# Performance work log

Measured on AMD Instinct MI355X. Metric: run time of the kernel, lower is better.

## Reference

```python
import jax, jax.numpy as jnp
import numpy as np

N_NODES = 50000
N_EDGES = 1000000
H_DIM = 128
OUT_DIM = 64
N_RELS = 16  # num_bases == num_rels


def setup_inputs() -> dict:
    key = jax.random.key(0)
    ks = jax.random.split(key, 12)
    node_ids = jnp.arange(N_NODES, dtype=jnp.int64) if jax.config.jax_enable_x64 else jnp.arange(N_NODES, dtype=jnp.int32)
    src = jax.random.randint(ks[0], (N_EDGES,), 0, N_NODES)
    dst = jax.random.randint(ks[1], (N_EDGES,), 0, N_NODES)
    etype = jax.random.randint(ks[2], (N_EDGES,), 0, N_RELS)
    norm = jax.random.uniform(ks[3], (N_EDGES, 1), dtype=jnp.float32)
    s1 = 1.0 / np.sqrt(H_DIM)
    s2 = 1.0 / np.sqrt(OUT_DIM)
    emb = jax.random.normal(ks[4], (N_NODES, H_DIM), dtype=jnp.float32)
    V1 = jax.random.normal(ks[5], (N_RELS, H_DIM, H_DIM), dtype=jnp.float32) * s1
    comp1 = jax.random.normal(ks[6], (N_RELS, N_RELS), dtype=jnp.float32) * (1.0 / np.sqrt(N_RELS))
    bias1 = jnp.zeros((H_DIM,), dtype=jnp.float32)
    V2 = jax.random.normal(ks[7], (N_RELS, H_DIM, OUT_DIM), dtype=jnp.float32) * s2
    comp2 = jax.random.normal(ks[8], (N_RELS, N_RELS), dtype=jnp.float32) * (1.0 / np.sqrt(N_RELS))
    bias2 = jnp.zeros((OUT_DIM,), dtype=jnp.float32)
    return {"node_ids": node_ids, "src": src, "dst": dst, "etype": etype, "norm": norm,
            "emb": emb, "V1": V1, "comp1": comp1, "bias1": bias1,
            "V2": V2, "comp2": comp2, "bias2": bias2}


def _rel_graph_conv(x, src, dst, etype, norm, V, comp, bias, num_nodes):
    # Basis decomposition: W_r = sum_b comp[r, b] * V_b  -> [R, in, out]
    W = jnp.einsum('rb,bio->rio', comp, V)
    # Per-relation transform of all nodes: [R, N, out]
    Y = jnp.einsum('ni,rio->rno', x, W)
    # Per-edge message: gather (etype, src) then scale by norm  -> [E, out]
    m = Y[etype, src] * norm
    # Scatter-add to destination nodes
    h = jax.ops.segment_sum(m, dst, num_segments=num_nodes)
    return h + bias


def reference(node_ids, src, dst, etype, norm, emb, V1, comp1, bias1, V2, comp2, bias2):
    x = emb[node_ids]  # [N, H]
    h = jax.nn.relu(_rel_graph_conv(x, src, dst, etype, norm, V1, comp1, bias1, x.shape[0]))
    h = _rel_graph_conv(h, src, dst, etype, norm, V2, comp2, bias2, x.shape[0])
    return h
```

## Files before the change

### kernel.cpp

```cpp
#include <hip/hip_runtime.h>


typedef short bf16x8 __attribute__((ext_vector_type(8)));
typedef float f32x4 __attribute__((ext_vector_type(4)));

#define RELS 16
#define HDIM 128
#define DSTBLK 66
#define MT_P 5
#define CHUNK 32
#define MAXBINS 12288

__device__ inline unsigned short f2bf(float f) {
  unsigned int u = __float_as_uint(f);
  unsigned int r = u + 0x7FFFu + ((u >> 16) & 1u);
  return (unsigned short)(r >> 16);
}

__global__ void cvt_bf16(const float* __restrict__ in, unsigned short* __restrict__ out, int n8) {
  int i = blockIdx.x * blockDim.x + threadIdx.x;
  if (i >= n8) return;
  float4 a = ((const float4*)in)[i * 2];
  float4 b = ((const float4*)in)[i * 2 + 1];
  uint4 o;
  o.x = (unsigned)f2bf(a.x) | ((unsigned)f2bf(a.y) << 16);
  o.y = (unsigned)f2bf(a.z) | ((unsigned)f2bf(a.w) << 16);
  o.z = (unsigned)f2bf(b.x) | ((unsigned)f2bf(b.y) << 16);
  o.w = (unsigned)f2bf(b.z) | ((unsigned)f2bf(b.w) << 16);
  ((uint4*)out)[i] = o;
}

__global__ void compute_w(const float* __restrict__ comp, const float* __restrict__ V,
                          unsigned short* __restrict__ Wt, int IO) {
  int idx = blockIdx.x * blockDim.x + threadIdx.x;
  if (idx >= RELS * IO * HDIM) return;
  int k = idx & (HDIM - 1);
  int o = (idx >> 7) % IO;
  int r = idx / (IO * HDIM);
  float s = 0.f;
#pragma unroll
  for (int b = 0; b < RELS; b++)
    s = fmaf(comp[r * RELS + b], V[(size_t)b * HDIM * IO + (size_t)k * IO + o], s);
  Wt[idx] = f2bf(s);
}

__global__ void hist_bins(const int* __restrict__ dst, const int* __restrict__ etype,
                          int n, int nbins, int* __restrict__ counts) {
  __shared__ int lh[MAXBINS];
  for (int j = threadIdx.x; j < nbins; j += blockDim.x) lh[j] = 0;
  __syncthreads();
  for (int i = blockIdx.x * blockDim.x + threadIdx.x; i < n; i += gridDim.x * blockDim.x)
    atomicAdd(&lh[(dst[i] / DSTBLK) * RELS + etype[i]], 1);
  __syncthreads();
  for (int j = threadIdx.x; j < nbins; j += blockDim.x) {
    int c = lh[j];
    if (c) atomicAdd(&counts[j], c);
  }
}

__global__ void scan_offsets(const int* __restrict__ counts, int* __restrict__ offsets, int nbins) {
  __shared__ int csum[256];
  const int t = threadIdx.x;
  const int CH = (nbins + 255) / 256;
  int lo = t * CH, hi = min(lo + CH, nbins);
  int s = 0;
  for (int i = lo; i < hi; i++) s += (counts[i] + 15) & ~15;
  csum[t] = s;
  __syncthreads();
#pragma unroll
  for (int d = 1; d < 256; d <<= 1) {
    int v = (t >= d) ? csum[t - d] : 0;
    __syncthreads();
    csum[t] += v;
    __syncthreads();
  }
  int run = (t == 0) ? 0 : csum[t - 1];
  for (int i = lo; i < hi; i++) {
    offsets[i] = run;
    run += (counts[i] + 15) & ~15;
  }
  if (lo < nbins && hi == nbins) offsets[nbins] = run;
}

__global__ void scatter_bins(const int* __restrict__ src, const int* __restrict__ dst,
                             const int* __restrict__ etype, const float* __restrict__ norm,
                             int n, const int* __restrict__ offsets, int* __restrict__ cursor,
                             uint2* __restrict__ ebuf) {
  for (int i = blockIdx.x * blockDim.x + threadIdx.x; i < n; i += gridDim.x * blockDim.x) {
    int d = dst[i];
    int blk = d / DSTBLK;
    int b = blk * RELS + etype[i];
    int p = offsets[b] + atomicAdd(&cursor[b], 1);
    ebuf[p] = make_uint2((unsigned)src[i] | ((unsigned)(d - blk * DSTBLK) << 20),
                         __float_as_uint(norm[i]));
  }
}

template <int OUT, bool BF16_RELU_OUT>
__launch_bounds__(256, 3)
__global__ void rgcn_layer(const unsigned short* __restrict__ Xb,
                           const unsigned short* __restrict__ Wt,
                           const uint2* __restrict__ ebuf,
                           const int* __restrict__ offsets, const int* __restrict__ counts,
                           const float* __restrict__ bias, void* __restrict__ Hout,
                           int nNodes) {
  constexpr int NT = OUT / 64;
  __shared__ __align__(16) unsigned short xs[2][CHUNK][136];
  __shared__ __align__(16) unsigned short ys[OUT][40];
  __shared__ __align__(16) unsigned short pmat[2][80][40];

  const int t = threadIdx.x;
  const int w = t >> 6;
  const int lane = t & 63;
  const int quad = lane >> 4;
  const int l16 = lane & 15;
  const int r0 = t >> 4;
  const int k8 = t & 15;
  const bool isHandler = (t & 7) == 0;
  const int myCol = t >> 3;
  const int nodeBase = blockIdx.x * DSTBLK;
  const int binBase = blockIdx.x * RELS;
  const int colBase = w * (OUT / 4);

  for (int i = t; i < 2 * CHUNK * 136 / 8; i += 256) ((uint4*)xs)[i] = make_uint4(0, 0, 0, 0);
  for (int i = t; i < OUT * 40 / 8; i += 256) ((uint4*)ys)[i] = make_uint4(0, 0, 0, 0);
  for (int i = t; i < 2 * 80 * 40 / 8; i += 256) ((uint4*)pmat)[i] = make_uint4(0, 0, 0, 0);

  f32x4 pacc[MT_P][NT] = {};

  int bin = 0, base = 0, binEnd = 0, realEnd = 0;
  for (; bin < RELS; bin++) {
    base = offsets[binBase + bin];
    binEnd = offsets[binBase + bin + 1];
    if (base < binEnd) { realEnd = base + counts[binBase + bin]; break; }
  }

  __syncthreads();

  int pdA = -1, pdB = -1;
  if (bin < RELS) {
    int nR = min(CHUNK, realEnd - base);
    if (r0 < nR) {
      uint2 e = ebuf[base + r0];
      *(uint4*)&xs[0][r0][k8 * 8] = *(const uint4*)(Xb + (size_t)(e.x & 0xFFFFFu) * HDIM + k8 * 8);
    }
    if (16 + r0 < nR) {
      uint2 e = ebuf[base + 16 + r0];
      *(uint4*)&xs[0][16 + r0][k8 * 8] = *(const uint4*)(Xb + (size_t)(e.x & 0xFFFFFu) * HDIM + k8 * 8);
    }
    if (isHandler && myCol < nR) {
      uint2 m = ebuf[base + myCol];
      int dl = (int)(m.x >> 20) & 127;
      pmat[0][dl][myCol] = f2bf(__uint_as_float(m.y));
      pdB = dl;
    }
  }
  __syncthreads();

  int cb = 0;
  int curRel = -1;
  bf16x8 wf[4][NT];

  while (bin < RELS) {
    const int nRows = min(CHUNK, realEnd - base);

    if (bin != curRel) {
      curRel = bin;
      const unsigned short* Wr = Wt + (size_t)bin * OUT * HDIM;
#pragma unroll
      for (int ks = 0; ks < 4; ks++)
#pragma unroll
        for (int nt = 0; nt < NT; nt++)
          wf[ks][nt] = *(const bf16x8*)(Wr + (size_t)(colBase + nt * 16 + l16) * HDIM + ks * 32 + quad * 8);
    }

    int nbin = bin, nbase = base + CHUNK, nbinEnd = binEnd, nrealEnd = realEnd;
    if (nbase >= binEnd) {
      for (nbin = bin + 1; nbin < RELS; nbin++) {
        nbase = offsets[binBase + nbin];
        nbinEnd = offsets[binBase + nbin + 1];
        if (nbase < nbinEnd) { nrealEnd = nbase + counts[binBase + nbin]; break; }
      }
    }
    const bool hasNext = nbin < RELS;
    const int nR = hasNext ? min(CHUNK, nrealEnd - nbase) : 0;

    uint2 e0, e1, em;
    if (hasNext) {
      if (r0 < nR) e0 = ebuf[nbase + r0];
      if (16 + r0 < nR) e1 = ebuf[nbase + 16 + r0];
      if (isHandler && myCol < nR) em = ebuf[nbase + myCol];
    }

#pragma unroll
    for (int mt = 0; mt < 2; mt++) {
      if (mt * 16 < nRows) {
        f32x4 dacc[NT] = {};
#pragma unroll
        for (int ks = 0; ks < 4; ks++) {
          bf16x8 a = *(const bf16x8*)&xs[cb][mt * 16 + l16][ks * 32 + quad * 8];
#pragma unroll
          for (int nt = 0; nt < NT; nt++)
            dacc[nt] = __builtin_amdgcn_mfma_f32_16x16x32_bf16(a, wf[ks][nt], dacc[nt], 0, 0, 0);
        }
#pragma unroll
        for (int nt = 0; nt < NT; nt++) {
          uint2 pk;
          pk.x = (unsigned)f2bf(dacc[nt][0]) | ((unsigned)f2bf(dacc[nt][1]) << 16);
          pk.y = (unsigned)f2bf(dacc[nt][2]) | ((unsigned)f2bf(dacc[nt][3]) << 16);
          *(uint2*)&ys[colBase + nt * 16 + l16][mt * 16 + quad * 4] = pk;
        }
      }
    }

    uint4 g0, g1;
    if (hasNext) {
      if (r0 < nR) g0 = *(const uint4*)(Xb + (size_t)(e0.x & 0xFFFFFu) * HDIM + k8 * 8);
      if (16 + r0 < nR) g1 = *(const uint4*)(Xb + (size_t)(e1.x & 0xFFFFFu) * HDIM + k8 * 8);
    }

    {
      bf16x8 bfv[NT];
#pragma unroll
      for (int nt = 0; nt < NT; nt++)
        bfv[nt] = *(const bf16x8*)&ys[colBase + nt * 16 + l16][quad * 8];
#pragma unroll
      for (int mt = 0; mt < MT_P; mt++) {
        bf16x8 a = *(const bf16x8*)&pmat[cb][mt * 16 + l16][quad * 8];
#pragma unroll
        for (int nt = 0; nt < NT; nt++)
          pacc[mt][nt] = __builtin_amdgcn_mfma_f32_16x16x32_bf16(a, bfv[nt], pacc[mt][nt], 0, 0, 0);
      }
    }

    if (hasNext) {
      if (r0 < nR) *(uint4*)&xs[cb ^ 1][r0][k8 * 8] = g0;
      if (16 + r0 < nR) *(uint4*)&xs[cb ^ 1][16 + r0][k8 * 8] = g1;
      if (isHandler) {
        if (pdA >= 0) pmat[cb ^ 1][pdA][myCol] = 0;
        if (myCol < nR) {
          int dl = (int)(em.x >> 20) & 127;
          pmat[cb ^ 1][dl][myCol] = f2bf(__uint_as_float(em.y));
          pdA = dl;
        } else {
          pdA = -1;
        }
      }
    }
    { int tmp = pdA; pdA = pdB; pdB = tmp; }

    if (hasNext) __syncthreads();

    bin = nbin; base = nbase; binEnd = nbinEnd; realEnd = nrealEnd;
    cb ^= 1;
  }

#pragma unroll
  for (int mt = 0; mt < MT_P; mt++) {
#pragma unroll
    for (int reg = 0; reg < 4; reg++) {
      int ld = mt * 16 + quad * 4 + reg;
      int node = nodeBase + ld;
      if (ld < DSTBLK && node < nNodes) {
#pragma unroll
        for (int nt = 0; nt < NT; nt++) {
          int col = colBase + nt * 16 + l16;
          float v = pacc[mt][nt][reg] + bias[col];
          if constexpr (BF16_RELU_OUT)
            ((unsigned short*)Hout)[(size_t)node * OUT + col] = f2bf(fmaxf(v, 0.f));
          else
            ((float*)Hout)[(size_t)node * OUT + col] = v;
        }
      }
    }
  }
}

extern "C" void kernel_launch(void* const* d_in, const int* in_sizes, int n_in,
                              void* d_out, int out_size, void* d_ws, size_t ws_size,
                              hipStream_t stream) {
  const int*   src   = (const int*)d_in[1];
  const int*   dst   = (const int*)d_in[2];
  const int*   etype = (const int*)d_in[3];
  const float* norm  = (const float*)d_in[4];
  const float* emb   = (const float*)d_in[5];
  const float* V1    = (const float*)d_in[6];
  const float* comp1 = (const float*)d_in[7];
  const float* bias1 = (const float*)d_in[8];
  const float* V2    = (const float*)d_in[9];
  const float* comp2 = (const float*)d_in[10];
  const float* bias2 = (const float*)d_in[11];
  float* out = (float*)d_out;

  const int N = in_sizes[0];
  const int E = in_sizes[1];
  const int H = 128, O = 64;
  const int NB = (N + DSTBLK - 1) / DSTBLK;
  const int NBINS = NB * RELS;
  const int EPAD_MAX = E + NBINS * 16;

  char* ws = (char*)d_ws;
  size_t off = 0;
  auto alloc = [&](size_t bytes) -> void* {
    void* p = ws + off;
    off += (bytes + 255) & ~(size_t)255;
    return p;
  };
  unsigned short* W1t  = (unsigned short*)alloc(sizeof(short) * RELS * H * H);
  unsigned short* W2t  = (unsigned short*)alloc(sizeof(short) * RELS * O * H);
  unsigned short* embh = (unsigned short*)alloc(sizeof(short) * (size_t)N * H);
  unsigned short* h1b  = (unsigned short*)alloc(sizeof(short) * (size_t)N * H);
  uint2* ebuf = (uint2*)alloc(sizeof(uint2) * EPAD_MAX);
  int* counts  = (int*)alloc(sizeof(int) * NBINS);
  int* cursor  = (int*)alloc(sizeof(int) * NBINS);
  int* offsets = (int*)alloc(sizeof(int) * (NBINS + 1));

  hipMemsetAsync(counts, 0, sizeof(int) * NBINS, stream);
  hipMemsetAsync(cursor, 0, sizeof(int) * NBINS, stream);

  cvt_bf16<<<((size_t)N * H / 8 + 255) / 256, 256, 0, stream>>>(emb, embh, N * H / 8);
  compute_w<<<(RELS * H * H + 255) / 256, 256, 0, stream>>>(comp1, V1, W1t, H);
  compute_w<<<(RELS * O * H + 255) / 256, 256, 0, stream>>>(comp2, V2, W2t, O);
  hist_bins<<<256, 256, 0, stream>>>(dst, etype, E, NBINS, counts);
  scan_offsets<<<1, 256, 0, stream>>>(counts, offsets, NBINS);
  scatter_bins<<<1024, 256, 0, stream>>>(src, dst, etype, norm, E, offsets, cursor, ebuf);

  rgcn_layer<128, true><<<NB, 256, 0, stream>>>(embh, W1t, ebuf, offsets, counts, bias1, (void*)h1b, N);
  rgcn_layer<64, false><<<NB, 256, 0, stream>>>(h1b, W2t, ebuf, offsets, counts, bias2, (void*)out, N);
}
```

Baseline: 460.8 us.

## Build norm matrix in registers, use power-of-two dst blocks, fuse weight kernels

Destination blocks shrink to 64 nodes so bin indices come from shifts, and the LDS-based per-block histogram becomes direct global atomics. The per-chunk norm matrix is no longer kept in shared memory: each lane loads packed edge records and builds the MFMA A fragment by comparing the destination slot with its row. The edge buffer is pre-filled with 0xFF so padding never matches, and norm is stored as bf16. The two weight-composition kernels are merged into one launch, and occupancy rises to 4 waves via launch bounds. The costs are an extra memset of the edge buffer, more ALU work per MFMA fragment, and more contention on global histogram atomics.

```diff
diff --git a/kernel.cpp b/kernel.cpp
--- a/kernel.cpp
+++ b/kernel.cpp
@@ -6,10 +6,9 @@
 
 #define RELS 16
 #define HDIM 128
-#define DSTBLK 66
-#define MT_P 5
+#define DSTBLK 64
+#define MT_P 4
 #define CHUNK 32
-#define MAXBINS 12288
 
 __device__ inline unsigned short f2bf(float f) {
   unsigned int u = __float_as_uint(f);
@@ -30,32 +29,36 @@
   ((uint4*)out)[i] = o;
 }
 
-__global__ void compute_w(const float* __restrict__ comp, const float* __restrict__ V,
-                          unsigned short* __restrict__ Wt, int IO) {
+__global__ void compute_w2(const float* __restrict__ comp1, const float* __restrict__ V1,
+                           const float* __restrict__ comp2, const float* __restrict__ V2,
+                           unsigned short* __restrict__ W1t, unsigned short* __restrict__ W2t) {
   int idx = blockIdx.x * blockDim.x + threadIdx.x;
-  if (idx >= RELS * IO * HDIM) return;
-  int k = idx & (HDIM - 1);
-  int o = (idx >> 7) % IO;
-  int r = idx / (IO * HDIM);
-  float s = 0.f;
-#pragma unroll
-  for (int b = 0; b < RELS; b++)
-    s = fmaf(comp[r * RELS + b], V[(size_t)b * HDIM * IO + (size_t)k * IO + o], s);
-  Wt[idx] = f2bf(s);
+  const int PER_R = HDIM * (HDIM + 64);
+  if (idx >= RELS * PER_R) return;
+  int r = idx / PER_R;
+  int rem = idx - r * PER_R;
+  if (rem < HDIM * HDIM) {
+    int o = rem >> 7, k = rem & 127;
+    float s = 0.f;
+#pragma unroll
+    for (int b = 0; b < RELS; b++)
+      s = fmaf(comp1[r * RELS + b], V1[(size_t)b * HDIM * HDIM + (size_t)k * HDIM + o], s);
+    W1t[(size_t)r * HDIM * HDIM + rem] = f2bf(s);
+  } else {
+    int rr = rem - HDIM * HDIM;
+    int o = rr >> 7, k = rr & 127;
+    float s = 0.f;
+#pragma unroll
+    for (int b = 0; b < RELS; b++)
+      s = fmaf(comp2[r * RELS + b], V2[(size_t)b * HDIM * 64 + (size_t)k * 64 + o], s);
+    W2t[(size_t)r * 64 * HDIM + rr] = f2bf(s);
+  }
 }
 
 __global__ void hist_bins(const int* __restrict__ dst, const int* __restrict__ etype,
-                          int n, int nbins, int* __restrict__ counts) {
-  __shared__ int lh[MAXBINS];
-  for (int j = threadIdx.x; j < nbins; j += blockDim.x) lh[j] = 0;
-  __syncthreads();
+                          int n, int* __restrict__ counts) {
   for (int i = blockIdx.x * blockDim.x + threadIdx.x; i < n; i += gridDim.x * blockDim.x)
-    atomicAdd(&lh[(dst[i] / DSTBLK) * RELS + etype[i]], 1);
-  __syncthreads();
-  for (int j = threadIdx.x; j < nbins; j += blockDim.x) {
-    int c = lh[j];
-    if (c) atomicAdd(&counts[j], c);
-  }
+    atomicAdd(&counts[(dst[i] >> 6) * RELS + etype[i]], 1);
 }
 
 __global__ void scan_offsets(const int* __restrict__ counts, int* __restrict__ offsets, int nbins) {
@@ -88,16 +91,15 @@
                              uint2* __restrict__ ebuf) {
   for (int i = blockIdx.x * blockDim.x + threadIdx.x; i < n; i += gridDim.x * blockDim.x) {
     int d = dst[i];
-    int blk = d / DSTBLK;
-    int b = blk * RELS + etype[i];
+    int b = (d >> 6) * RELS + etype[i];
     int p = offsets[b] + atomicAdd(&cursor[b], 1);
-    ebuf[p] = make_uint2((unsigned)src[i] | ((unsigned)(d - blk * DSTBLK) << 20),
-                         __float_as_uint(norm[i]));
+    ebuf[p] = make_uint2((unsigned)src[i] | ((unsigned)(d & 63) << 20),
+                         (unsigned)f2bf(norm[i]));
   }
 }
 
 template <int OUT, bool BF16_RELU_OUT>
-__launch_bounds__(256, 3)
+__launch_bounds__(256, 4)
 __global__ void rgcn_layer(const unsigned short* __restrict__ Xb,
                            const unsigned short* __restrict__ Wt,
                            const uint2* __restrict__ ebuf,
@@ -107,7 +109,6 @@
   constexpr int NT = OUT / 64;
   __shared__ __align__(16) unsigned short xs[2][CHUNK][136];
   __shared__ __align__(16) unsigned short ys[OUT][40];
-  __shared__ __align__(16) unsigned short pmat[2][80][40];
 
   const int t = threadIdx.x;
   const int w = t >> 6;
@@ -116,15 +117,15 @@
   const int l16 = lane & 15;
   const int r0 = t >> 4;
   const int k8 = t & 15;
-  const bool isHandler = (t & 7) == 0;
-  const int myCol = t >> 3;
   const int nodeBase = blockIdx.x * DSTBLK;
   const int binBase = blockIdx.x * RELS;
   const int colBase = w * (OUT / 4);
 
+  {
+    uint4* yz = (uint4*)&ys[colBase][0];
+    for (int i = lane; i < (OUT / 4) * 5; i += 64) yz[i] = make_uint4(0, 0, 0, 0);
+  }
   for (int i = t; i < 2 * CHUNK * 136 / 8; i += 256) ((uint4*)xs)[i] = make_uint4(0, 0, 0, 0);
-  for (int i = t; i < OUT * 40 / 8; i += 256) ((uint4*)ys)[i] = make_uint4(0, 0, 0, 0);
-  for (int i = t; i < 2 * 80 * 40 / 8; i += 256) ((uint4*)pmat)[i] = make_uint4(0, 0, 0, 0);
 
   f32x4 pacc[MT_P][NT] = {};
 
@@ -137,7 +138,6 @@
 
   __syncthreads();
 
-  int pdA = -1, pdB = -1;
   if (bin < RELS) {
     int nR = min(CHUNK, realEnd - base);
     if (r0 < nR) {
@@ -148,12 +148,6 @@
       uint2 e = ebuf[base + 16 + r0];
       *(uint4*)&xs[0][16 + r0][k8 * 8] = *(const uint4*)(Xb + (size_t)(e.x & 0xFFFFFu) * HDIM + k8 * 8);
     }
-    if (isHandler && myCol < nR) {
-      uint2 m = ebuf[base + myCol];
-      int dl = (int)(m.x >> 20) & 127;
-      pmat[0][dl][myCol] = f2bf(__uint_as_float(m.y));
-      pdB = dl;
-    }
   }
   __syncthreads();
 
@@ -163,6 +157,14 @@
 
   while (bin < RELS) {
     const int nRows = min(CHUNK, realEnd - base);
+    const int avail = binEnd - base;
+
+    uint4 q01, q23, q45, q67;
+    {
+      const uint4* eb = (const uint4*)(ebuf + base + quad * 8);
+      if (quad * 8 < avail) { q01 = eb[0]; q23 = eb[1]; q45 = eb[2]; q67 = eb[3]; }
+      else q01 = q23 = q45 = q67 = make_uint4(~0u, ~0u, ~0u, ~0u);
+    }
 
     if (bin != curRel) {
       curRel = bin;
@@ -185,11 +187,10 @@
     const bool hasNext = nbin < RELS;
     const int nR = hasNext ? min(CHUNK, nrealEnd - nbase) : 0;
 
-    uint2 e0, e1, em;
+    uint2 e0, e1;
     if (hasNext) {
       if (r0 < nR) e0 = ebuf[nbase + r0];
       if (16 + r0 < nR) e1 = ebuf[nbase + 16 + r0];
-      if (isHandler && myCol < nR) em = ebuf[nbase + myCol];
     }
 
 #pragma unroll
@@ -226,30 +227,27 @@
         bfv[nt] = *(const bf16x8*)&ys[colBase + nt * 16 + l16][quad * 8];
 #pragma unroll
       for (int mt = 0; mt < MT_P; mt++) {
-        bf16x8 a = *(const bf16x8*)&pmat[cb][mt * 16 + l16][quad * 8];
+        const unsigned tgt = (unsigned)(mt * 16 + l16);
+        union { unsigned u[4]; bf16x8 v; } pf;
+        pf.u[0] = ((((q01.x >> 20) & 127u) == tgt) ? (q01.y & 0xFFFFu) : 0u) |
+                  (((((q01.z >> 20) & 127u) == tgt) ? (q01.w & 0xFFFFu) : 0u) << 16);
+        pf.u[1] = ((((q23.x >> 20) & 127u) == tgt) ? (q23.y & 0xFFFFu) : 0u) |
+                  (((((q23.z >> 20) & 127u) == tgt) ? (q23.w & 0xFFFFu) : 0u) << 16);
+        pf.u[2] = ((((q45.x >> 20) & 127u) == tgt) ? (q45.y & 0xFFFFu) : 0u) |
+                  (((((q45.z >> 20) & 127u) == tgt) ? (q45.w & 0xFFFFu) : 0u) << 16);
+        pf.u[3] = ((((q67.x >> 20) & 127u) == tgt) ? (q67.y & 0xFFFFu) : 0u) |
+                  (((((q67.z >> 20) & 127u) == tgt) ? (q67.w & 0xFFFFu) : 0u) << 16);
 #pragma unroll
         for (int nt = 0; nt < NT; nt++)
-          pacc[mt][nt] = __builtin_amdgcn_mfma_f32_16x16x32_bf16(a, bfv[nt], pacc[mt][nt], 0, 0, 0);
+          pacc[mt][nt] = __builtin_amdgcn_mfma_f32_16x16x32_bf16(pf.v, bfv[nt], pacc[mt][nt], 0, 0, 0);
       }
     }
 
     if (hasNext) {
       if (r0 < nR) *(uint4*)&xs[cb ^ 1][r0][k8 * 8] = g0;
       if (16 + r0 < nR) *(uint4*)&xs[cb ^ 1][16 + r0][k8 * 8] = g1;
-      if (isHandler) {
-        if (pdA >= 0) pmat[cb ^ 1][pdA][myCol] = 0;
-        if (myCol < nR) {
-          int dl = (int)(em.x >> 20) & 127;
-          pmat[cb ^ 1][dl][myCol] = f2bf(__uint_as_float(em.y));
-          pdA = dl;
-        } else {
-          pdA = -1;
-        }
-      }
-    }
-    { int tmp = pdA; pdA = pdB; pdB = tmp; }
-
-    if (hasNext) __syncthreads();
+      __syncthreads();
+    }
 
     bin = nbin; base = nbase; binEnd = nbinEnd; realEnd = nrealEnd;
     cb ^= 1;
@@ -259,9 +257,8 @@
   for (int mt = 0; mt < MT_P; mt++) {
 #pragma unroll
     for (int reg = 0; reg < 4; reg++) {
-      int ld = mt * 16 + quad * 4 + reg;
-      int node = nodeBase + ld;
-      if (ld < DSTBLK && node < nNodes) {
+      int node = nodeBase + mt * 16 + quad * 4 + reg;
+      if (node < nNodes) {
 #pragma unroll
         for (int nt = 0; nt < NT; nt++) {
           int col = colBase + nt * 16 + l16;
@@ -297,7 +294,7 @@
   const int H = 128, O = 64;
   const int NB = (N + DSTBLK - 1) / DSTBLK;
   const int NBINS = NB * RELS;
-  const int EPAD_MAX = E + NBINS * 16;
+  const int EPAD_MAX = E + NBINS * 16 + 64;
 
   char* ws = (char*)d_ws;
   size_t off = 0;
@@ -317,11 +314,11 @@
 
   hipMemsetAsync(counts, 0, sizeof(int) * NBINS, stream);
   hipMemsetAsync(cursor, 0, sizeof(int) * NBINS, stream);
+  hipMemsetAsync(ebuf, 0xFF, sizeof(uint2) * EPAD_MAX, stream);
 
   cvt_bf16<<<((size_t)N * H / 8 + 255) / 256, 256, 0, stream>>>(emb, embh, N * H / 8);
-  compute_w<<<(RELS * H * H + 255) / 256, 256, 0, stream>>>(comp1, V1, W1t, H);
-  compute_w<<<(RELS * O * H + 255) / 256, 256, 0, stream>>>(comp2, V2, W2t, O);
-  hist_bins<<<256, 256, 0, stream>>>(dst, etype, E, NBINS, counts);
+  compute_w2<<<(RELS * H * (H + O) + 255) / 256, 256, 0, stream>>>(comp1, V1, comp2, V2, W1t, W2t);
+  hist_bins<<<512, 256, 0, stream>>>(dst, etype, E, counts);
   scan_offsets<<<1, 256, 0, stream>>>(counts, offsets, NBINS);
   scatter_bins<<<1024, 256, 0, stream>>>(src, dst, etype, norm, E, offsets, cursor, ebuf);
 
```

Result: slower. 536.4 us (+16.4%).
